# Performance work log

Hardware: AMD Instinct MI355X
Metric: run time of the kernel (lower is better)

The kernel has to match this reference:

```python
import jax, jax.numpy as jnp
import numpy as np
from jax.scipy.linalg import expm

N_QUBITS = 10
DIM = 2 ** N_QUBITS        # 1024, statevector dimension
N_GATES = 24
FEAT_LEN = 1000            # padded with zeros up to DIM (pad_with=0.0)


def setup_inputs() -> dict:
    key = jax.random.key(0)
    kf, kt, kr, ki = jax.random.split(key, 4)
    feature = jax.random.normal(kf, (FEAT_LEN,), dtype=jnp.float32)
    # theta param: (len(gate_indices), 1) as in nn.param('theta', ..., (K, 1))
    theta = jax.random.normal(kt, (N_GATES, 1), dtype=jnp.float32)
    # fixed ansatz generators (Hermitian after symmetrization in reference)
    gens_re = jax.random.normal(kr, (N_GATES, DIM, DIM), dtype=jnp.float32)
    gens_im = jax.random.normal(ki, (N_GATES, DIM, DIM), dtype=jnp.float32)
    return {"feature": feature, "theta": theta, "gens_re": gens_re, "gens_im": gens_im}


def reference(feature, theta, gens_re, gens_im):
    D = gens_re.shape[-1]
    # Hermitian generators G_k = (M + M^H)/2
    M = gens_re.astype(jnp.complex64) + 1j * gens_im.astype(jnp.complex64)
    G = 0.5 * (M + jnp.conj(jnp.swapaxes(M, -1, -2)))  # [K, D, D]

    # AmplitudeEmbedding: pad feature with zeros to D, then L2-normalize
    psi = jnp.zeros((D,), dtype=jnp.complex64)
    psi = psi.at[: feature.shape[0]].set(feature.astype(jnp.complex64))
    psi = psi / jnp.linalg.norm(psi)

    # U_k = expm(-1j * theta_k * G_k), batched over gates
    coeff = (-1j) * theta[:, 0].astype(jnp.complex64)  # [K]
    U = jax.vmap(expm)(coeff[:, None, None] * G)       # [K, D, D]

    # sequential application of gates to the state
    def step(p, Uk):
        return Uk @ p, None

    psi, _ = jax.lax.scan(step, psi, U)

    # qml.probs over all wires
    probs = jnp.abs(psi) ** 2
    return probs
```

## Files before the change

### kernel.cpp

```cpp
#include <hip/hip_runtime.h>
#include <math.h>

#define DIM      1024
#define K_GATES  24
#define NMAX     512
#define QUAD_M   2048
#define BBOUND   66.0f
#define ROWS     16
#define NBLOCKS  64
#define NTHREADS 1024

__device__ __forceinline__ float2 cohLoad(const float2* p) {
    unsigned long long v = __hip_atomic_load((const unsigned long long*)p,
                                             __ATOMIC_RELAXED, __HIP_MEMORY_SCOPE_AGENT);
    union { unsigned long long u; float2 f; } c; c.u = v; return c.f;
}
__device__ __forceinline__ void cohStore(float2* p, float2 val) {
    union { unsigned long long u; float2 f; } c; c.f = val;
    __hip_atomic_store((unsigned long long*)p, c.u,
                       __ATOMIC_RELAXED, __HIP_MEMORY_SCOPE_AGENT);
}

__global__ __launch_bounds__(1024) void init_state(const float* __restrict__ f,
                                                   int nfeat, float2* __restrict__ xbuf,
                                                   unsigned int* __restrict__ bar) {
    __shared__ float red[16];
    __shared__ float invn_s;
    int t = threadIdx.x;
    float v = (t < nfeat) ? f[t] : 0.f;
    float s = v * v;
    #pragma unroll
    for (int o = 1; o < 64; o <<= 1) s += __shfl_xor(s, o);
    if ((t & 63) == 0) red[t >> 6] = s;
    __syncthreads();
    if (t == 0) {
        float tot = 0.f;
        for (int i = 0; i < 16; i++) tot += red[i];
        invn_s = 1.0f / sqrtf(tot);
        *bar = 0u;
    }
    __syncthreads();
    xbuf[t] = make_float2(v * invn_s, 0.f);
}

__global__ __launch_bounds__(256) void bessel_coef(const float* __restrict__ theta,
                                                   float2* __restrict__ coefs) {
    int n = blockIdx.x;
    int k = blockIdx.y;
    double tau = (double)theta[k] * (double)BBOUND;
    int t = threadIdx.x;
    double acc = 0.0;
    #pragma unroll
    for (int i = 0; i < QUAD_M / 256; i++) {
        int j = t + 256 * i;
        double phi = (2.0 * M_PI / (double)QUAD_M) * (double)j;
        acc += cos((double)n * phi - tau * sin(phi));
    }
    #pragma unroll
    for (int o = 1; o < 64; o <<= 1) acc += __shfl_xor(acc, o);
    __shared__ double red[4];
    if ((t & 63) == 0) red[t >> 6] = acc;
    __syncthreads();
    if (t == 0) {
        double J = (red[0] + red[1] + red[2] + red[3]) / (double)QUAD_M;
        double f = (n == 0) ? 1.0 : 2.0;
        float cr = 0.f, cim = 0.f;
        switch (n & 3) {
            case 0: cr  =  (float)(f * J); break;
            case 1: cim = -(float)(f * J); break;
            case 2: cr  = -(float)(f * J); break;
            case 3: cim =  (float)(f * J); break;
        }
        coefs[k * NMAX + n] = make_float2(cr, cim);
    }
}

__global__ __launch_bounds__(NMAX) void trunc_len(const float2* __restrict__ coefs,
                                                  int* __restrict__ nterm) {
    int k = blockIdx.x;
    int t = threadIdx.x;
    float2 c = coefs[k * NMAX + t];
    float mag = fabsf(c.x) + fabsf(c.y);
    int myn = (mag > 5e-7f) ? t : 0;
    #pragma unroll
    for (int o = 1; o < 64; o <<= 1) myn = max(myn, __shfl_xor(myn, o));
    __shared__ int red[8];
    if ((t & 63) == 0) red[t >> 6] = myn;
    __syncthreads();
    if (t == 0) {
        int m = 1;
        for (int i = 0; i < 8; i++) m = max(m, red[i]);
        nterm[k] = min(m, NMAX - 1);
    }
}

__global__ __launch_bounds__(NTHREADS) void evolve(const float* __restrict__ gre,
                                                   const float* __restrict__ gim,
                                                   float2* __restrict__ xbuf,
                                                   const float2* __restrict__ coefs,
                                                   const int* __restrict__ nterm,
                                                   unsigned int* __restrict__ bar,
                                                   float* __restrict__ out) {
    __shared__ float2 Gs[ROWS * DIM];
    __shared__ float2 xs[DIM];
    const int t = threadIdx.x, b = blockIdx.x;
    const int wave = t >> 6, lane = t & 63;
    const int r0 = b * ROWS;
    const int r = r0 + wave;
    const float hB = 0.5f / BBOUND;

    int cur = 0;
    int eps = 0;
    float2 acc = make_float2(0.f, 0.f);

    auto gbar = [&]() {
        eps++;
        __syncthreads();
        if (t == 0) {
            __hip_atomic_fetch_add(bar, 1u, __ATOMIC_RELAXED, __HIP_MEMORY_SCOPE_AGENT);
            unsigned tgt = (unsigned)eps * NBLOCKS;
            while (__hip_atomic_load(bar, __ATOMIC_RELAXED, __HIP_MEMORY_SCOPE_AGENT) < tgt)
                __builtin_amdgcn_s_sleep(4);
        }
        __syncthreads();
    };

    for (int k = 0; k < K_GATES; k++) {
        const float* R = gre + (size_t)k * DIM * DIM;
        const float* I = gim + (size_t)k * DIM * DIM;

        {
            const float4* Rc = (const float4*)(R + (size_t)t * DIM + r0);
            const float4* Ic = (const float4*)(I + (size_t)t * DIM + r0);
            float4 ra0 = Rc[0], ra1 = Rc[1], ra2 = Rc[2], ra3 = Rc[3];
            float4 ia0 = Ic[0], ia1 = Ic[1], ia2 = Ic[2], ia3 = Ic[3];
            Gs[ 0 * DIM + t] = make_float2(hB * ra0.x, -hB * ia0.x);
            Gs[ 1 * DIM + t] = make_float2(hB * ra0.y, -hB * ia0.y);
            Gs[ 2 * DIM + t] = make_float2(hB * ra0.z, -hB * ia0.z);
            Gs[ 3 * DIM + t] = make_float2(hB * ra0.w, -hB * ia0.w);
            Gs[ 4 * DIM + t] = make_float2(hB * ra1.x, -hB * ia1.x);
            Gs[ 5 * DIM + t] = make_float2(hB * ra1.y, -hB * ia1.y);
            Gs[ 6 * DIM + t] = make_float2(hB * ra1.z, -hB * ia1.z);
            Gs[ 7 * DIM + t] = make_float2(hB * ra1.w, -hB * ia1.w);
            Gs[ 8 * DIM + t] = make_float2(hB * ra2.x, -hB * ia2.x);
            Gs[ 9 * DIM + t] = make_float2(hB * ra2.y, -hB * ia2.y);
            Gs[10 * DIM + t] = make_float2(hB * ra2.z, -hB * ia2.z);
            Gs[11 * DIM + t] = make_float2(hB * ra2.w, -hB * ia2.w);
            Gs[12 * DIM + t] = make_float2(hB * ra3.x, -hB * ia3.x);
            Gs[13 * DIM + t] = make_float2(hB * ra3.y, -hB * ia3.y);
            Gs[14 * DIM + t] = make_float2(hB * ra3.z, -hB * ia3.z);
            Gs[15 * DIM + t] = make_float2(hB * ra3.w, -hB * ia3.w);
        }
        __syncthreads();
        {
            const float4* Rr = (const float4*)(R + (size_t)r * DIM);
            const float4* Ir = (const float4*)(I + (size_t)r * DIM);
            float4* G4 = (float4*)(Gs + (size_t)wave * DIM);
            #pragma unroll
            for (int m = 0; m < 4; m++) {
                int i4 = lane + 64 * m;
                float4 rv = Rr[i4], iv = Ir[i4];
                float4 g0 = G4[2 * i4], g1 = G4[2 * i4 + 1];
                g0.x += hB * rv.x; g0.y += hB * iv.x;
                g0.z += hB * rv.y; g0.w += hB * iv.y;
                g1.x += hB * rv.z; g1.y += hB * iv.z;
                g1.z += hB * rv.w; g1.w += hB * iv.w;
                G4[2 * i4] = g0; G4[2 * i4 + 1] = g1;
            }
        }
        __syncthreads();

        const int N = nterm[k];
        const float2* C = coefs + (size_t)k * NMAX;

        float2 t_prev, t_cur;
        bool first = true;

        for (int n = 1; n <= N; n++) {
            xs[t] = cohLoad(&xbuf[cur * DIM + t]);
            __syncthreads();

            float sre = 0.f, sim = 0.f;
            {
                const float4* x4 = (const float4*)xs;
                const float4* g4 = (const float4*)(Gs + (size_t)wave * DIM);
                #pragma unroll
                for (int m = 0; m < 8; m++) {
                    int idx = lane + 64 * m;
                    float4 xv = x4[idx];
                    float4 gv = g4[idx];
                    sre += gv.x * xv.x - gv.y * xv.y + gv.z * xv.z - gv.w * xv.w;
                    sim += gv.x * xv.y + gv.y * xv.x + gv.z * xv.w + gv.w * xv.z;
                }
                #pragma unroll
                for (int o = 1; o < 64; o <<= 1) {
                    sre += __shfl_xor(sre, o);
                    sim += __shfl_xor(sim, o);
                }
            }
            float2 w = make_float2(sre, sim);

            float2 t_next;
            if (first) {
                t_prev = xs[r];
                t_next = w;
                float2 c0 = C[0], c1 = C[1];
                acc.x = c0.x * t_prev.x - c0.y * t_prev.y + c1.x * w.x - c1.y * w.y;
                acc.y = c0.x * t_prev.y + c0.y * t_prev.x + c1.x * w.y + c1.y * w.x;
                first = false;
            } else {
                t_next = make_float2(2.f * w.x - t_prev.x, 2.f * w.y - t_prev.y);
                float2 cn = C[n];
                acc.x += cn.x * t_next.x - cn.y * t_next.y;
                acc.y += cn.x * t_next.y + cn.y * t_next.x;
                t_prev = t_cur;
            }
            t_cur = t_next;

            if (lane == 0) cohStore(&xbuf[(cur ^ 1) * DIM + r], t_next);
            cur ^= 1;
            gbar();
        }

        if (lane == 0) cohStore(&xbuf[(cur ^ 1) * DIM + r], acc);
        cur ^= 1;
        gbar();
    }

    if (lane == 0) out[r] = acc.x * acc.x + acc.y * acc.y;
}

extern "C" void kernel_launch(void* const* d_in, const int* in_sizes, int n_in,
                              void* d_out, int out_size, void* d_ws, size_t ws_size,
                              hipStream_t stream) {
    const float* feat  = (const float*)d_in[0];
    const float* theta = (const float*)d_in[1];
    const float* gre   = (const float*)d_in[2];
    const float* gim   = (const float*)d_in[3];

    char* base = (char*)d_ws;
    float2*       xbuf  = (float2*)base;
    float2*       coefs = (float2*)(base + 2 * DIM * sizeof(float2));
    int*          nterm = (int*)(base + 2 * DIM * sizeof(float2)
                                 + K_GATES * NMAX * sizeof(float2));
    unsigned int* bar   = (unsigned int*)(base + 2 * DIM * sizeof(float2)
                                          + K_GATES * NMAX * sizeof(float2)
                                          + K_GATES * sizeof(int));
    float* outp = (float*)d_out;

    init_state<<<1, 1024, 0, stream>>>(feat, in_sizes[0], xbuf, bar);
    bessel_coef<<<dim3(NMAX, K_GATES), 256, 0, stream>>>(theta, coefs);
    trunc_len<<<K_GATES, NMAX, 0, stream>>>(coefs, nterm);

    void* args[] = {(void*)&gre, (void*)&gim, (void*)&xbuf,
                    (void*)&coefs, (void*)&nterm, (void*)&bar, (void*)&outp};
    hipLaunchCooperativeKernel((void*)evolve, dim3(NBLOCKS), dim3(NTHREADS),
                               args, 0, stream);
}
```

Baseline: 6.499 ms.

## Replace grid barrier with epoch-tagged per-element dataflow flags

Drops the atomic-counter grid barrier. Each state element is now stored as a 64-bit word holding the value in the low half and an epoch tag in the high half. Readers spin on their own elements until the tag matches the current epoch, so a block waits only for the data it needs rather than for every block to arrive at a counter. The final accumulator write is folded into the last Chebyshev step, removing one sync epoch per gate. The risk is that leftover tags from a previous launch in the odd buffer are not cleared by init, so different inputs across calls could in principle race with stale values.

```diff
diff --git a/kernel.cpp b/kernel.cpp
--- a/kernel.cpp
+++ b/kernel.cpp
@@ -10,20 +10,15 @@
 #define NBLOCKS  64
 #define NTHREADS 1024
 
-__device__ __forceinline__ float2 cohLoad(const float2* p) {
-    unsigned long long v = __hip_atomic_load((const unsigned long long*)p,
-                                             __ATOMIC_RELAXED, __HIP_MEMORY_SCOPE_AGENT);
-    union { unsigned long long u; float2 f; } c; c.u = v; return c.f;
-}
-__device__ __forceinline__ void cohStore(float2* p, float2 val) {
-    union { unsigned long long u; float2 f; } c; c.f = val;
-    __hip_atomic_store((unsigned long long*)p, c.u,
-                       __ATOMIC_RELAXED, __HIP_MEMORY_SCOPE_AGENT);
+__device__ __forceinline__ void tagStore(unsigned long long* p, float v, unsigned e) {
+    unsigned long long w = ((unsigned long long)e << 32) | (unsigned long long)__float_as_uint(v);
+    __hip_atomic_store(p, w, __ATOMIC_RELAXED, __HIP_MEMORY_SCOPE_AGENT);
 }
 
 __global__ __launch_bounds__(1024) void init_state(const float* __restrict__ f,
-                                                   int nfeat, float2* __restrict__ xbuf,
-                                                   unsigned int* __restrict__ bar) {
+                                                   int nfeat,
+                                                   unsigned long long* __restrict__ wre,
+                                                   unsigned long long* __restrict__ wim) {
     __shared__ float red[16];
     __shared__ float invn_s;
     int t = threadIdx.x;
@@ -37,10 +32,10 @@
         float tot = 0.f;
         for (int i = 0; i < 16; i++) tot += red[i];
         invn_s = 1.0f / sqrtf(tot);
-        *bar = 0u;
-    }
-    __syncthreads();
-    xbuf[t] = make_float2(v * invn_s, 0.f);
+    }
+    __syncthreads();
+    tagStore(&wre[t], v * invn_s, 0u);
+    tagStore(&wim[t], 0.f, 0u);
 }
 
 __global__ __launch_bounds__(256) void bessel_coef(const float* __restrict__ theta,
@@ -96,10 +91,10 @@
 
 __global__ __launch_bounds__(NTHREADS) void evolve(const float* __restrict__ gre,
                                                    const float* __restrict__ gim,
-                                                   float2* __restrict__ xbuf,
+                                                   unsigned long long* __restrict__ wre,
+                                                   unsigned long long* __restrict__ wim,
                                                    const float2* __restrict__ coefs,
                                                    const int* __restrict__ nterm,
-                                                   unsigned int* __restrict__ bar,
                                                    float* __restrict__ out) {
     __shared__ float2 Gs[ROWS * DIM];
     __shared__ float2 xs[DIM];
@@ -109,21 +104,9 @@
     const int r = r0 + wave;
     const float hB = 0.5f / BBOUND;
 
-    int cur = 0;
-    int eps = 0;
+    unsigned e = 0;
     float2 acc = make_float2(0.f, 0.f);
 
-    auto gbar = [&]() {
-        eps++;
-        __syncthreads();
-        if (t == 0) {
-            __hip_atomic_fetch_add(bar, 1u, __ATOMIC_RELAXED, __HIP_MEMORY_SCOPE_AGENT);
-            unsigned tgt = (unsigned)eps * NBLOCKS;
-            while (__hip_atomic_load(bar, __ATOMIC_RELAXED, __HIP_MEMORY_SCOPE_AGENT) < tgt)
-                __builtin_amdgcn_s_sleep(4);
-        }
-        __syncthreads();
-    };
 
     for (int k = 0; k < K_GATES; k++) {
         const float* R = gre + (size_t)k * DIM * DIM;
@@ -177,7 +160,19 @@
         bool first = true;
 
         for (int n = 1; n <= N; n++) {
-            xs[t] = cohLoad(&xbuf[cur * DIM + t]);
+            {
+                const unsigned long long* pre = wre + (size_t)(e & 1) * DIM + t;
+                const unsigned long long* pim = wim + (size_t)(e & 1) * DIM + t;
+                unsigned long long a, bw;
+                for (;;) {
+                    a  = __hip_atomic_load(pre, __ATOMIC_RELAXED, __HIP_MEMORY_SCOPE_AGENT);
+                    bw = __hip_atomic_load(pim, __ATOMIC_RELAXED, __HIP_MEMORY_SCOPE_AGENT);
+                    if (((unsigned)(a >> 32) == e) & ((unsigned)(bw >> 32) == e)) break;
+                    __builtin_amdgcn_s_sleep(1);
+                }
+                xs[t] = make_float2(__uint_as_float((unsigned)a),
+                                    __uint_as_float((unsigned)bw));
+            }
             __syncthreads();
 
             float sre = 0.f, sim = 0.f;
@@ -217,14 +212,17 @@
             }
             t_cur = t_next;
 
-            if (lane == 0) cohStore(&xbuf[(cur ^ 1) * DIM + r], t_next);
-            cur ^= 1;
-            gbar();
-        }
-
-        if (lane == 0) cohStore(&xbuf[(cur ^ 1) * DIM + r], acc);
-        cur ^= 1;
-        gbar();
+            {
+                float2 val = (n == N) ? acc : t_next;
+                unsigned ne = e + 1;
+                if (lane == 0) {
+                    tagStore(wre + (size_t)(ne & 1) * DIM + r, val.x, ne);
+                    tagStore(wim + (size_t)(ne & 1) * DIM + r, val.y, ne);
+                }
+            }
+            __syncthreads();
+            e++;
+        }
     }
 
     if (lane == 0) out[r] = acc.x * acc.x + acc.y * acc.y;
@@ -239,21 +237,18 @@
     const float* gim   = (const float*)d_in[3];
 
     char* base = (char*)d_ws;
-    float2*       xbuf  = (float2*)base;
-    float2*       coefs = (float2*)(base + 2 * DIM * sizeof(float2));
-    int*          nterm = (int*)(base + 2 * DIM * sizeof(float2)
-                                 + K_GATES * NMAX * sizeof(float2));
-    unsigned int* bar   = (unsigned int*)(base + 2 * DIM * sizeof(float2)
-                                          + K_GATES * NMAX * sizeof(float2)
-                                          + K_GATES * sizeof(int));
+    unsigned long long* wre   = (unsigned long long*)base;
+    unsigned long long* wim   = (unsigned long long*)(base + 2 * DIM * 8);
+    float2*             coefs = (float2*)(base + 4 * DIM * 8);
+    int*                nterm = (int*)(base + 4 * DIM * 8 + K_GATES * NMAX * sizeof(float2));
     float* outp = (float*)d_out;
 
-    init_state<<<1, 1024, 0, stream>>>(feat, in_sizes[0], xbuf, bar);
+    init_state<<<1, 1024, 0, stream>>>(feat, in_sizes[0], wre, wim);
     bessel_coef<<<dim3(NMAX, K_GATES), 256, 0, stream>>>(theta, coefs);
     trunc_len<<<K_GATES, NMAX, 0, stream>>>(coefs, nterm);
 
-    void* args[] = {(void*)&gre, (void*)&gim, (void*)&xbuf,
-                    (void*)&coefs, (void*)&nterm, (void*)&bar, (void*)&outp};
+    void* args[] = {(void*)&gre, (void*)&gim, (void*)&wre, (void*)&wim,
+                    (void*)&coefs, (void*)&nterm, (void*)&outp};
     hipLaunchCooperativeKernel((void*)evolve, dim3(NBLOCKS), dim3(NTHREADS),
                                args, 0, stream);
 }
```

After: 6.605 ms. Within noise of the previous version (+1.6%).
